# Kernel tuning notes

Measured on AMD Instinct MI355X. Metric: run time of the kernel, lower is better.

Reference implementation:

```python
import jax, jax.numpy as jnp
import numpy as np

N = 20000       # nodes
E = 640000      # random edges (self-loops appended -> E + N total)
G = 64          # graphs in batch
F_IN = 114
H1 = 3          # heads in layer 1
D2 = 128        # output_dim of layer 2
NEG = 0.2       # GATConv leaky_relu negative slope


def setup_inputs() -> dict:
    key = jax.random.key(0)
    ks = jax.random.split(key, 20)
    x = jax.random.normal(ks[0], (N, F_IN), jnp.float32)
    src = jax.random.randint(ks[1], (E,), 0, N, jnp.int32)
    dst = jax.random.randint(ks[2], (E,), 0, N, jnp.int32)
    loop = jnp.arange(N, dtype=jnp.int32)  # PyG add_self_loops=True
    edge_index = jnp.stack([jnp.concatenate([src, loop]),
                            jnp.concatenate([dst, loop])])
    batch = (jnp.arange(N) * G // N).astype(jnp.int32)  # every graph non-empty

    def lin(k, i, o):
        return jax.random.normal(k, (i, o), jnp.float32) * (1.0 / np.sqrt(i))

    return {
        "x": x, "edge_index": edge_index, "batch": batch,
        # GATConv 1: 114 -> 114 per head, 3 heads, concat
        "W1": lin(ks[3], F_IN, H1 * F_IN),
        "a_src1": jax.random.normal(ks[4], (H1, F_IN), jnp.float32) * 0.1,
        "a_dst1": jax.random.normal(ks[5], (H1, F_IN), jnp.float32) * 0.1,
        "b1": jnp.zeros((H1 * F_IN,), jnp.float32),
        # GATConv 2: 342 -> 128, 1 head
        "W2": lin(ks[6], H1 * F_IN, D2),
        "a_src2": jax.random.normal(ks[7], (1, D2), jnp.float32) * 0.1,
        "a_dst2": jax.random.normal(ks[8], (1, D2), jnp.float32) * 0.1,
        "b2": jnp.zeros((D2,), jnp.float32),
        # MLP head
        "Wg": lin(ks[9], D2, 64),  "bg": jnp.zeros((64,), jnp.float32),
        "Wf1": lin(ks[10], 64, 32), "bf1": jnp.zeros((32,), jnp.float32),
        "Wf2": lin(ks[11], 32, 16), "bf2": jnp.zeros((16,), jnp.float32),
        "Wo": lin(ks[12], 16, 1),   "bo": jnp.zeros((1,), jnp.float32),
    }


def gat_conv(x, edge_index, W, a_src, a_dst, b, heads, dim):
    """PyG GATConv (self-loops already in edge_index, eval mode)."""
    n = x.shape[0]
    h = (x @ W).reshape(n, heads, dim)             # [N,H,D]
    src, dst = edge_index[0], edge_index[1]
    alpha_s = jnp.sum(h * a_src, axis=-1)          # [N,H]
    alpha_d = jnp.sum(h * a_dst, axis=-1)          # [N,H]
    e = jax.nn.leaky_relu(alpha_s[src] + alpha_d[dst], NEG)  # [E,H]
    # segment softmax over destination nodes
    m = jax.ops.segment_max(e, dst, num_segments=n)
    ex = jnp.exp(e - m[dst])
    s = jax.ops.segment_sum(ex, dst, num_segments=n)
    alpha = ex / s[dst]                            # [E,H]
    out = jax.ops.segment_sum(h[src] * alpha[..., None], dst, num_segments=n)
    return out.reshape(n, heads * dim) + b


def reference(x, edge_index, batch, W1, a_src1, a_dst1, b1,
              W2, a_src2, a_dst2, b2, Wg, bg, Wf1, bf1, Wf2, bf2, Wo, bo):
    h = jax.nn.elu(gat_conv(x, edge_index, W1, a_src1, a_dst1, b1, H1, F_IN))
    h = jax.nn.relu(gat_conv(h, edge_index, W2, a_src2, a_dst2, b2, 1, D2))
    g = jax.ops.segment_max(h, batch, num_segments=G)   # global max pool [G,128]
    g = jax.nn.relu(g @ Wg + bg)
    g = jax.nn.relu(g @ Wf1 + bf1)
    g = jax.nn.relu(g @ Wf2 + bf2)
    return g @ Wo + bo                                  # [G,1]
```

## Files before the change

### kernel.cpp

```cpp
#include <hip/hip_runtime.h>

#define NN 20000
#define EE 660000
#define GG 64
#define FIN 114
#define H1 3
#define F1 342
#define D2 128
#define NEG 0.2f

__device__ inline unsigned fenc(float f) {
    unsigned u = __float_as_uint(f);
    return (u & 0x80000000u) ? ~u : (u | 0x80000000u);
}
__device__ inline float fdec(unsigned u) {
    return (u & 0x80000000u) ? __uint_as_float(u & 0x7FFFFFFFu) : __uint_as_float(~u);
}
__device__ inline float lrelu(float x) { return x > 0.f ? x : NEG * x; }

__global__ void k_wa(const float* __restrict__ W1, const float* __restrict__ aS,
                     const float* __restrict__ aD, float* __restrict__ was,
                     float* __restrict__ wad) {
    int tid = blockIdx.x * 256 + threadIdx.x;
    if (tid >= 2 * FIN * H1) return;
    int which = tid >= FIN * H1;
    int i = which ? tid - FIN * H1 : tid;
    int k = i / H1, h = i % H1;
    const float* a = which ? aD : aS;
    float s = 0.f;
    for (int d = 0; d < FIN; d++) s += W1[k * F1 + h * FIN + d] * a[h * FIN + d];
    (which ? wad : was)[i] = s;
}

__global__ void k_prep1(const float* __restrict__ W1, float* __restrict__ W1P) {
    int tid = blockIdx.x * 256 + threadIdx.x;
    if (tid >= H1 * 128 * 128) return;
    int h = tid / (128 * 128);
    int rem = tid & (128 * 128 - 1);
    int k = rem >> 7, c = rem & 127;
    W1P[tid] = (c < FIN && k < FIN) ? W1[k * F1 + h * FIN + c] : 0.f;
}

__global__ void k_prep2(const float* __restrict__ W2, float* __restrict__ W2P) {
    int tid = blockIdx.x * 256 + threadIdx.x;
    if (tid >= 3 * 128 * 128) return;
    int hk = tid >> 7, c = tid & 127;
    int h = hk >> 7, k = hk & 127;
    W2P[tid] = (k < FIN) ? W2[(h * FIN + k) * D2 + c] : 0.f;
}

__global__ __launch_bounds__(256) void k_alpha1x(const float* __restrict__ x,
                                                 const float* __restrict__ was,
                                                 const float* __restrict__ wad,
                                                 float* __restrict__ as1,
                                                 float* __restrict__ ad1) {
    int n = blockIdx.x * 4 + (threadIdx.x >> 6);
    int l = threadIdx.x & 63;
    if (n >= NN) return;
    float x0 = x[n * FIN + l];
    float x1 = (l < FIN - 64) ? x[n * FIN + 64 + l] : 0.f;
    float s[H1], d[H1];
#pragma unroll
    for (int h = 0; h < H1; h++) {
        float w0s = was[l * H1 + h], w0d = wad[l * H1 + h];
        float w1s = (l < FIN - 64) ? was[(64 + l) * H1 + h] : 0.f;
        float w1d = (l < FIN - 64) ? wad[(64 + l) * H1 + h] : 0.f;
        s[h] = x0 * w0s + x1 * w1s;
        d[h] = x0 * w0d + x1 * w1d;
    }
#pragma unroll
    for (int o = 32; o > 0; o >>= 1) {
#pragma unroll
        for (int h = 0; h < H1; h++) {
            s[h] += __shfl_down(s[h], o);
            d[h] += __shfl_down(d[h], o);
        }
    }
    if (l == 0) {
#pragma unroll
        for (int h = 0; h < H1; h++) {
            as1[n * H1 + h] = s[h];
            ad1[n * H1 + h] = d[h];
        }
    }
}

__global__ void k_count(const int* __restrict__ dst, int* __restrict__ cnt) {
    int e = blockIdx.x * 256 + threadIdx.x;
    if (e < EE) atomicAdd(&cnt[dst[e]], 1);
}

__global__ __launch_bounds__(1024) void k_scan(const int* __restrict__ cnt,
                                               int* __restrict__ off) {
    __shared__ int part[1024];
    int t = threadIdx.x;
    const int CH = 20;
    int loc[CH];
    int s = 0;
    int base = t * CH;
    for (int i = 0; i < CH; i++) {
        int idx = base + i;
        int v = (idx < NN) ? cnt[idx] : 0;
        loc[i] = s;
        s += v;
    }
    part[t] = s;
    __syncthreads();
    for (int d = 1; d < 1024; d <<= 1) {
        int v = (t >= d) ? part[t - d] : 0;
        __syncthreads();
        part[t] += v;
        __syncthreads();
    }
    int pre = (t == 0) ? 0 : part[t - 1];
    for (int i = 0; i < CH; i++) {
        int idx = base + i;
        if (idx < NN) off[idx] = pre + loc[i];
    }
    if (t == 1023) off[NN] = part[1023];
}

__global__ void k_scatter(const int* __restrict__ src, const int* __restrict__ dst,
                          const int* __restrict__ off, int* __restrict__ cur,
                          int* __restrict__ csr_src) {
    int e = blockIdx.x * 256 + threadIdx.x;
    if (e < EE) {
        int d = dst[e];
        int pos = off[d] + atomicAdd(&cur[d], 1);
        csr_src[pos] = src[e];
    }
}

__global__ __launch_bounds__(128) void k_aggx(const float* __restrict__ x,
                                              const float* __restrict__ as1,
                                              const float* __restrict__ ad1,
                                              const int* __restrict__ off,
                                              const int* __restrict__ csr_src,
                                              float* __restrict__ xaggP) {
    int n = blockIdx.x, t = threadIdx.x;
    int e0 = off[n], e1 = off[n + 1];
    float adv0 = ad1[n * H1 + 0], adv1 = ad1[n * H1 + 1], adv2 = ad1[n * H1 + 2];
    __shared__ int ssrc[64];
    __shared__ float sw[64][H1];
    __shared__ float red[64][H1];
    float acc0 = 0.f, acc1 = 0.f, acc2 = 0.f;
    float ps0 = 0.f, ps1 = 0.f, ps2 = 0.f;
    for (int base = e0; base < e1; base += 64) {
        int c = min(64, e1 - base);
        __syncthreads();
        if (t < c) {
            int s = csr_src[base + t];
            ssrc[t] = s;
            float w0 = __expf(lrelu(as1[s * H1 + 0] + adv0));
            float w1 = __expf(lrelu(as1[s * H1 + 1] + adv1));
            float w2 = __expf(lrelu(as1[s * H1 + 2] + adv2));
            sw[t][0] = w0; sw[t][1] = w1; sw[t][2] = w2;
            ps0 += w0; ps1 += w1; ps2 += w2;
        }
        __syncthreads();
        if (t < FIN) {
            for (int j = 0; j < c; j++) {
                float xv = x[ssrc[j] * FIN + t];
                acc0 += xv * sw[j][0];
                acc1 += xv * sw[j][1];
                acc2 += xv * sw[j][2];
            }
        }
    }
    __syncthreads();
    if (t < 64) { red[t][0] = ps0; red[t][1] = ps1; red[t][2] = ps2; }
    __syncthreads();
    for (int sr = 32; sr > 0; sr >>= 1) {
        if (t < sr) {
            red[t][0] += red[t + sr][0];
            red[t][1] += red[t + sr][1];
            red[t][2] += red[t + sr][2];
        }
        __syncthreads();
    }
    float i0 = 1.f / red[0][0], i1 = 1.f / red[0][1], i2 = 1.f / red[0][2];
    float v0 = (t < FIN) ? acc0 * i0 : 0.f;
    float v1 = (t < FIN) ? acc1 * i1 : 0.f;
    float v2 = (t < FIN) ? acc2 * i2 : 0.f;
    xaggP[(size_t)0 * NN * 128 + n * 128 + t] = v0;
    xaggP[(size_t)1 * NN * 128 + n * 128 + t] = v1;
    xaggP[(size_t)2 * NN * 128 + n * 128 + t] = v2;
}

__global__ __launch_bounds__(256) void k_gemm1t(const float* __restrict__ xaggP,
                                                const float* __restrict__ W1P,
                                                const float* __restrict__ b1,
                                                float* __restrict__ h1aP) {
    int h = blockIdx.y;
    int rb = blockIdx.x * 64;
    int t = threadIdx.x;
    int tr = t >> 4, tc = t & 15;
    __shared__ float As[64][36];
    __shared__ float Bs[32][132];
    const float* Ap = xaggP + (size_t)h * NN * 128;
    const float* Bp = W1P + (size_t)h * 128 * 128;
    const float4 zf4 = make_float4(0.f, 0.f, 0.f, 0.f);

    int ar0 = t >> 3, ak0 = t & 7;
    int ar1 = 32 + ar0;
    int bk[4], bn[4];
#pragma unroll
    for (int q = 0; q < 4; q++) { int idd = t + q * 256; bk[q] = idd >> 5; bn[q] = idd & 31; }

    float4 aR[2], bR[4];
    {
        int g0 = rb + ar0, g1 = rb + ar1;
        aR[0] = (g0 < NN) ? *(const float4*)(Ap + (size_t)g0 * 128 + ak0 * 4) : zf4;
        aR[1] = (g1 < NN) ? *(const float4*)(Ap + (size_t)g1 * 128 + ak0 * 4) : zf4;
#pragma unroll
        for (int q = 0; q < 4; q++)
            bR[q] = *(const float4*)(Bp + (size_t)bk[q] * 128 + bn[q] * 4);
    }
    float acc[4][8] = {};
    for (int tile = 0; tile < 4; tile++) {
        if (tile) __syncthreads();
        *(float4*)(&As[ar0][ak0 * 4]) = aR[0];
        *(float4*)(&As[ar1][ak0 * 4]) = aR[1];
#pragma unroll
        for (int q = 0; q < 4; q++) *(float4*)(&Bs[bk[q]][bn[q] * 4]) = bR[q];
        __syncthreads();
        if (tile < 3) {
            int k0 = (tile + 1) * 32;
            int g0 = rb + ar0, g1 = rb + ar1;
            aR[0] = (g0 < NN) ? *(const float4*)(Ap + (size_t)g0 * 128 + k0 + ak0 * 4) : zf4;
            aR[1] = (g1 < NN) ? *(const float4*)(Ap + (size_t)g1 * 128 + k0 + ak0 * 4) : zf4;
#pragma unroll
            for (int q = 0; q < 4; q++)
                bR[q] = *(const float4*)(Bp + (size_t)(k0 + bk[q]) * 128 + bn[q] * 4);
        }
#pragma unroll
        for (int kc = 0; kc < 32; kc += 4) {
            float a4[4][4];
#pragma unroll
            for (int r = 0; r < 4; r++)
                *(float4*)a4[r] = *(const float4*)(&As[tr * 4 + r][kc]);
#pragma unroll
            for (int kk = 0; kk < 4; kk++) {
                float4 b0 = *(const float4*)(&Bs[kc + kk][tc * 4]);
                float4 b1v = *(const float4*)(&Bs[kc + kk][64 + tc * 4]);
#pragma unroll
                for (int r = 0; r < 4; r++) {
                    float av = a4[r][kk];
                    acc[r][0] += av * b0.x;  acc[r][1] += av * b0.y;
                    acc[r][2] += av * b0.z;  acc[r][3] += av * b0.w;
                    acc[r][4] += av * b1v.x; acc[r][5] += av * b1v.y;
                    acc[r][6] += av * b1v.z; acc[r][7] += av * b1v.w;
                }
            }
        }
    }
    float* Hp = h1aP + (size_t)h * NN * 128;
    int c0 = tc * 4, c1 = 64 + tc * 4;
    float bvA[4], bvB[4];
#pragma unroll
    for (int j = 0; j < 4; j++) {
        bvA[j] = b1[h * FIN + c0 + j];
        bvB[j] = (c1 + j < FIN) ? b1[h * FIN + c1 + j] : 0.f;
    }
#pragma unroll
    for (int r = 0; r < 4; r++) {
        int row = rb + tr * 4 + r;
        if (row >= NN) continue;
        float vA[4], vB[4];
#pragma unroll
        for (int j = 0; j < 4; j++) {
            float v = acc[r][j] + bvA[j];
            vA[j] = v > 0.f ? v : expm1f(v);
            float w = acc[r][j + 4] + bvB[j];
            vB[j] = (c1 + j < FIN) ? (w > 0.f ? w : expm1f(w)) : 0.f;
        }
        *(float4*)(Hp + (size_t)row * 128 + c0) = make_float4(vA[0], vA[1], vA[2], vA[3]);
        *(float4*)(Hp + (size_t)row * 128 + c1) = make_float4(vB[0], vB[1], vB[2], vB[3]);
    }
}

__global__ __launch_bounds__(256) void k_gemm2t(const float* __restrict__ h1aP,
                                                const float* __restrict__ W2P,
                                                float* __restrict__ h2) {
    int mt = blockIdx.x >> 1, nb = (blockIdx.x & 1) * 64;
    int rb = mt * 64;
    int t = threadIdx.x;
    int tr = t >> 4, tc = t & 15;
    __shared__ float As[64][36];
    __shared__ float Bs[32][68];
    const float4 zf4 = make_float4(0.f, 0.f, 0.f, 0.f);
    int ar0 = t >> 3, ak0 = t & 7;
    int ar1 = 32 + ar0;
    int bk0 = t >> 4, bn0 = t & 15;
    int bk1 = 16 + bk0;
    auto loadA = [&](int row, int kg) -> float4 {
        if (row >= NN) return zf4;
        int h = kg >> 7, kc = kg & 127;
        return *(const float4*)(h1aP + ((size_t)h * NN + row) * 128 + kc);
    };
    float4 aR[2], bR[2];
    {
        int g0 = rb + ar0, g1 = rb + ar1;
        aR[0] = loadA(g0, ak0 * 4);
        aR[1] = loadA(g1, ak0 * 4);
        bR[0] = *(const float4*)(W2P + (size_t)bk0 * D2 + nb + bn0 * 4);
        bR[1] = *(const float4*)(W2P + (size_t)bk1 * D2 + nb + bn0 * 4);
    }
    float acc[4][4] = {};
    for (int tile = 0; tile < 12; tile++) {
        if (tile) __syncthreads();
        *(float4*)(&As[ar0][ak0 * 4]) = aR[0];
        *(float4*)(&As[ar1][ak0 * 4]) = aR[1];
        *(float4*)(&Bs[bk0][bn0 * 4]) = bR[0];
        *(float4*)(&Bs[bk1][bn0 * 4]) = bR[1];
        __syncthreads();
        if (tile < 11) {
            int k0 = (tile + 1) * 32;
            int g0 = rb + ar0, g1 = rb + ar1;
            aR[0] = loadA(g0, k0 + ak0 * 4);
            aR[1] = loadA(g1, k0 + ak0 * 4);
            bR[0] = *(const float4*)(W2P + (size_t)(k0 + bk0) * D2 + nb + bn0 * 4);
            bR[1] = *(const float4*)(W2P + (size_t)(k0 + bk1) * D2 + nb + bn0 * 4);
        }
#pragma unroll
        for (int kc = 0; kc < 32; kc += 4) {
            float a4[4][4];
#pragma unroll
            for (int r = 0; r < 4; r++)
                *(float4*)a4[r] = *(const float4*)(&As[tr * 4 + r][kc]);
#pragma unroll
            for (int kk = 0; kk < 4; kk++) {
                float4 b0 = *(const float4*)(&Bs[kc + kk][tc * 4]);
#pragma unroll
                for (int r = 0; r < 4; r++) {
                    float av = a4[r][kk];
                    acc[r][0] += av * b0.x; acc[r][1] += av * b0.y;
                    acc[r][2] += av * b0.z; acc[r][3] += av * b0.w;
                }
            }
        }
    }
#pragma unroll
    for (int r = 0; r < 4; r++) {
        int row = rb + tr * 4 + r;
        if (row < NN)
            *(float4*)(&h2[(size_t)row * D2 + nb + tc * 4]) =
                make_float4(acc[r][0], acc[r][1], acc[r][2], acc[r][3]);
    }
}

__global__ __launch_bounds__(256) void k_alpha2(const float* __restrict__ h2,
                                                const float* __restrict__ aS,
                                                const float* __restrict__ aD,
                                                float* __restrict__ as2,
                                                float* __restrict__ ad2) {
    int n = blockIdx.x * 4 + (threadIdx.x >> 6);
    int l = threadIdx.x & 63;
    if (n >= NN) return;
    float v0 = h2[(size_t)n * D2 + l], v1 = h2[(size_t)n * D2 + 64 + l];
    float ps = v0 * aS[l] + v1 * aS[64 + l];
    float pd = v0 * aD[l] + v1 * aD[64 + l];
    for (int o = 32; o > 0; o >>= 1) {
        ps += __shfl_down(ps, o);
        pd += __shfl_down(pd, o);
    }
    if (l == 0) {
        as2[n] = ps;
        ad2[n] = pd;
    }
}

__global__ __launch_bounds__(128) void k_agg2f(const float* __restrict__ h2,
                                               const float* __restrict__ as2,
                                               const float* __restrict__ ad2,
                                               const int* __restrict__ off,
                                               const int* __restrict__ csr_src,
                                               const float* __restrict__ b2,
                                               unsigned* __restrict__ poolbuf) {
    int n = blockIdx.x, t = threadIdx.x;
    int e0 = off[n], e1 = off[n + 1];
    float adv = ad2[n];
    __shared__ int ssrc[64];
    __shared__ float sw[64];
    __shared__ float red[64];
    float acc = 0.f, ps = 0.f;
    for (int base = e0; base < e1; base += 64) {
        int c = min(64, e1 - base);
        __syncthreads();
        if (t < c) {
            int s = csr_src[base + t];
            ssrc[t] = s;
            float w = __expf(lrelu(as2[s] + adv));
            sw[t] = w;
            ps += w;
        }
        __syncthreads();
        for (int j = 0; j < c; j++) acc += h2[(size_t)ssrc[j] * D2 + t] * sw[j];
    }
    __syncthreads();
    if (t < 64) red[t] = ps;
    __syncthreads();
    for (int sr = 32; sr > 0; sr >>= 1) {
        if (t < sr) red[t] += red[t + sr];
        __syncthreads();
    }
    float v = fmaxf(acc / red[0] + b2[t], 0.f);
    int g = (int)(((long long)n * GG) / NN);
    atomicMax(&poolbuf[g * D2 + t], fenc(v));
}

__global__ __launch_bounds__(128) void k_mlp(const unsigned* __restrict__ poolbuf,
                                             const float* __restrict__ Wg,
                                             const float* __restrict__ bg,
                                             const float* __restrict__ Wf1,
                                             const float* __restrict__ bf1,
                                             const float* __restrict__ Wf2,
                                             const float* __restrict__ bf2,
                                             const float* __restrict__ Wo,
                                             const float* __restrict__ bo,
                                             float* __restrict__ out) {
    int g = blockIdx.x;
    int t = threadIdx.x;
    __shared__ float pool[D2];
    __shared__ float a1[64];
    __shared__ float a2[32];
    __shared__ float a3[16];
    pool[t] = fdec(poolbuf[g * D2 + t]);
    __syncthreads();
    if (t < 64) {
        float acc = bg[t];
        for (int k = 0; k < D2; k++) acc += pool[k] * Wg[k * 64 + t];
        a1[t] = fmaxf(acc, 0.f);
    }
    __syncthreads();
    if (t < 32) {
        float acc = bf1[t];
        for (int k = 0; k < 64; k++) acc += a1[k] * Wf1[k * 32 + t];
        a2[t] = fmaxf(acc, 0.f);
    }
    __syncthreads();
    if (t < 16) {
        float acc = bf2[t];
        for (int k = 0; k < 32; k++) acc += a2[k] * Wf2[k * 16 + t];
        a3[t] = fmaxf(acc, 0.f);
    }
    __syncthreads();
    if (t == 0) {
        float acc = bo[0];
        for (int k = 0; k < 16; k++) acc += a3[k] * Wo[k];
        out[g] = acc;
    }
}

extern "C" void kernel_launch(void* const* d_in, const int* in_sizes, int n_in,
                              void* d_out, int out_size, void* d_ws, size_t ws_size,
                              hipStream_t stream) {
    const float* x = (const float*)d_in[0];
    const int* ei = (const int*)d_in[1];
    const float* W1 = (const float*)d_in[3];
    const float* aS1 = (const float*)d_in[4];
    const float* aD1 = (const float*)d_in[5];
    const float* b1 = (const float*)d_in[6];
    const float* W2 = (const float*)d_in[7];
    const float* aS2 = (const float*)d_in[8];
    const float* aD2 = (const float*)d_in[9];
    const float* b2 = (const float*)d_in[10];
    const float* Wg = (const float*)d_in[11];
    const float* bg = (const float*)d_in[12];
    const float* Wf1 = (const float*)d_in[13];
    const float* bf1 = (const float*)d_in[14];
    const float* Wf2 = (const float*)d_in[15];
    const float* bf2 = (const float*)d_in[16];
    const float* Wo = (const float*)d_in[17];
    const float* bo = (const float*)d_in[18];
    float* out = (float*)d_out;

    const int* src = ei;
    const int* dst = ei + EE;

    char* ws = (char*)d_ws;
    size_t o = 0;
    auto alloc = [&](size_t bytes) -> char* {
        char* p = ws + o;
        o += (bytes + 255) & ~(size_t)255;
        return p;
    };
    float* was = (float*)alloc((size_t)FIN * H1 * 4);
    float* wad = (float*)alloc((size_t)FIN * H1 * 4);
    float* W1P = (float*)alloc((size_t)H1 * 128 * 128 * 4);
    float* W2P = (float*)alloc((size_t)3 * 128 * 128 * 4);
    float* as1 = (float*)alloc((size_t)NN * H1 * 4);
    float* ad1 = (float*)alloc((size_t)NN * H1 * 4);
    int* cnt = (int*)alloc((size_t)NN * 4);
    int* off = (int*)alloc((size_t)(NN + 1) * 4);
    int* cur = (int*)alloc((size_t)NN * 4);
    int* csr_src = (int*)alloc((size_t)EE * 4);
    float* xaggP = (float*)alloc((size_t)H1 * NN * 128 * 4);
    float* h1aP = (float*)alloc((size_t)H1 * NN * 128 * 4);
    float* h2 = (float*)alloc((size_t)NN * D2 * 4);
    float* as2 = (float*)alloc((size_t)NN * 4);
    float* ad2 = (float*)alloc((size_t)NN * 4);
    unsigned* poolbuf = (unsigned*)alloc((size_t)GG * D2 * 4);
    (void)ws_size;

    hipMemsetAsync(cnt, 0, (size_t)NN * 4, stream);
    hipMemsetAsync(cur, 0, (size_t)NN * 4, stream);
    hipMemsetAsync(poolbuf, 0, (size_t)GG * D2 * 4, stream);

    const int EB = (EE + 255) / 256;

    k_wa<<<(2 * FIN * H1 + 255) / 256, 256, 0, stream>>>(W1, aS1, aD1, was, wad);
    k_prep1<<<(H1 * 128 * 128 + 255) / 256, 256, 0, stream>>>(W1, W1P);
    k_prep2<<<(3 * 128 * 128 + 255) / 256, 256, 0, stream>>>(W2, W2P);
    k_alpha1x<<<(NN + 3) / 4, 256, 0, stream>>>(x, was, wad, as1, ad1);
    k_count<<<EB, 256, 0, stream>>>(dst, cnt);
    k_scan<<<1, 1024, 0, stream>>>(cnt, off);
    k_scatter<<<EB, 256, 0, stream>>>(src, dst, off, cur, csr_src);
    k_aggx<<<NN, 128, 0, stream>>>(x, as1, ad1, off, csr_src, xaggP);
    k_gemm1t<<<dim3((NN + 63) / 64, H1), 256, 0, stream>>>(xaggP, W1P, b1, h1aP);
    k_gemm2t<<<((NN + 63) / 64) * 2, 256, 0, stream>>>(h1aP, W2P, h2);
    k_alpha2<<<(NN + 3) / 4, 256, 0, stream>>>(h2, aS2, aD2, as2, ad2);
    k_agg2f<<<NN, 128, 0, stream>>>(h2, as2, ad2, off, csr_src, b2, poolbuf);
    k_mlp<<<GG, 128, 0, stream>>>(poolbuf, Wg, bg, Wf1, bf1, Wf2, bf2, Wo, bo, out);
}
```

Before: 317.4 us.

## Use 8x8 register tiles in GEMMs and split-K the second GEMM

Both dense GEMMs move to 128-thread blocks in which each thread computes an 8x8 output tile. The A tile is stored transposed in shared memory so a row fragment can be read with vector loads. The second GEMM now covers the full 128 output columns per block and splits K into two halves, writing two partial outputs. k_alpha2 sums those partials into h2 before computing the attention logits. The aim is more FMAs per shared-memory load, at the cost of extra partial-buffer traffic, higher register pressure and fewer threads per block.

```diff
diff --git a/kernel.cpp b/kernel.cpp
--- a/kernel.cpp
+++ b/kernel.cpp
@@ -187,7 +187,7 @@
     xaggP[(size_t)2 * NN * 128 + n * 128 + t] = v2;
 }
 
-__global__ __launch_bounds__(256) void k_gemm1t(const float* __restrict__ xaggP,
+__global__ __launch_bounds__(128) void k_gemm1n(const float* __restrict__ xaggP,
                                                 const float* __restrict__ W1P,
                                                 const float* __restrict__ b1,
                                                 float* __restrict__ h1aP) {
@@ -195,169 +195,167 @@
     int rb = blockIdx.x * 64;
     int t = threadIdx.x;
     int tr = t >> 4, tc = t & 15;
-    __shared__ float As[64][36];
-    __shared__ float Bs[32][132];
+    __shared__ float As[16][68];
+    __shared__ float Bs[16][132];
     const float* Ap = xaggP + (size_t)h * NN * 128;
     const float* Bp = W1P + (size_t)h * 128 * 128;
     const float4 zf4 = make_float4(0.f, 0.f, 0.f, 0.f);
-
-    int ar0 = t >> 3, ak0 = t & 7;
-    int ar1 = 32 + ar0;
-    int bk[4], bn[4];
-#pragma unroll
-    for (int q = 0; q < 4; q++) { int idd = t + q * 256; bk[q] = idd >> 5; bn[q] = idd & 31; }
-
+    int ar = t >> 1, aks = (t & 1) * 8;
+    int bkr = t >> 3, bnc = (t & 7) * 16;
     float4 aR[2], bR[4];
     {
-        int g0 = rb + ar0, g1 = rb + ar1;
-        aR[0] = (g0 < NN) ? *(const float4*)(Ap + (size_t)g0 * 128 + ak0 * 4) : zf4;
-        aR[1] = (g1 < NN) ? *(const float4*)(Ap + (size_t)g1 * 128 + ak0 * 4) : zf4;
+        int g = rb + ar;
+        aR[0] = (g < NN) ? *(const float4*)(Ap + (size_t)g * 128 + aks) : zf4;
+        aR[1] = (g < NN) ? *(const float4*)(Ap + (size_t)g * 128 + aks + 4) : zf4;
 #pragma unroll
         for (int q = 0; q < 4; q++)
-            bR[q] = *(const float4*)(Bp + (size_t)bk[q] * 128 + bn[q] * 4);
-    }
-    float acc[4][8] = {};
-    for (int tile = 0; tile < 4; tile++) {
+            bR[q] = *(const float4*)(Bp + (size_t)bkr * 128 + bnc + q * 4);
+    }
+    float acc[8][8] = {};
+    for (int tile = 0; tile < 8; tile++) {
         if (tile) __syncthreads();
-        *(float4*)(&As[ar0][ak0 * 4]) = aR[0];
-        *(float4*)(&As[ar1][ak0 * 4]) = aR[1];
-#pragma unroll
-        for (int q = 0; q < 4; q++) *(float4*)(&Bs[bk[q]][bn[q] * 4]) = bR[q];
-        __syncthreads();
-        if (tile < 3) {
-            int k0 = (tile + 1) * 32;
-            int g0 = rb + ar0, g1 = rb + ar1;
-            aR[0] = (g0 < NN) ? *(const float4*)(Ap + (size_t)g0 * 128 + k0 + ak0 * 4) : zf4;
-            aR[1] = (g1 < NN) ? *(const float4*)(Ap + (size_t)g1 * 128 + k0 + ak0 * 4) : zf4;
+#pragma unroll
+        for (int j = 0; j < 4; j++) {
+            As[aks + j][ar] = ((const float*)&aR[0])[j];
+            As[aks + 4 + j][ar] = ((const float*)&aR[1])[j];
+        }
+#pragma unroll
+        for (int q = 0; q < 4; q++) *(float4*)(&Bs[bkr][bnc + q * 4]) = bR[q];
+        __syncthreads();
+        if (tile < 7) {
+            int k0 = (tile + 1) * 16;
+            int g = rb + ar;
+            aR[0] = (g < NN) ? *(const float4*)(Ap + (size_t)g * 128 + k0 + aks) : zf4;
+            aR[1] = (g < NN) ? *(const float4*)(Ap + (size_t)g * 128 + k0 + aks + 4) : zf4;
 #pragma unroll
             for (int q = 0; q < 4; q++)
-                bR[q] = *(const float4*)(Bp + (size_t)(k0 + bk[q]) * 128 + bn[q] * 4);
-        }
-#pragma unroll
-        for (int kc = 0; kc < 32; kc += 4) {
-            float a4[4][4];
-#pragma unroll
-            for (int r = 0; r < 4; r++)
-                *(float4*)a4[r] = *(const float4*)(&As[tr * 4 + r][kc]);
-#pragma unroll
-            for (int kk = 0; kk < 4; kk++) {
-                float4 b0 = *(const float4*)(&Bs[kc + kk][tc * 4]);
-                float4 b1v = *(const float4*)(&Bs[kc + kk][64 + tc * 4]);
-#pragma unroll
-                for (int r = 0; r < 4; r++) {
-                    float av = a4[r][kk];
-                    acc[r][0] += av * b0.x;  acc[r][1] += av * b0.y;
-                    acc[r][2] += av * b0.z;  acc[r][3] += av * b0.w;
-                    acc[r][4] += av * b1v.x; acc[r][5] += av * b1v.y;
-                    acc[r][6] += av * b1v.z; acc[r][7] += av * b1v.w;
-                }
-            }
+                bR[q] = *(const float4*)(Bp + (size_t)(k0 + bkr) * 128 + bnc + q * 4);
+        }
+#pragma unroll
+        for (int k = 0; k < 16; k++) {
+            float a8[8], b8[8];
+            *(float4*)(a8 + 0) = *(const float4*)(&As[k][tr * 8]);
+            *(float4*)(a8 + 4) = *(const float4*)(&As[k][tr * 8 + 4]);
+            *(float4*)(b8 + 0) = *(const float4*)(&Bs[k][tc * 4]);
+            *(float4*)(b8 + 4) = *(const float4*)(&Bs[k][64 + tc * 4]);
+#pragma unroll
+            for (int r = 0; r < 8; r++)
+#pragma unroll
+                for (int j = 0; j < 8; j++) acc[r][j] += a8[r] * b8[j];
         }
     }
     float* Hp = h1aP + (size_t)h * NN * 128;
     int c0 = tc * 4, c1 = 64 + tc * 4;
-    float bvA[4], bvB[4];
+    float bv[8];
 #pragma unroll
     for (int j = 0; j < 4; j++) {
-        bvA[j] = b1[h * FIN + c0 + j];
-        bvB[j] = (c1 + j < FIN) ? b1[h * FIN + c1 + j] : 0.f;
-    }
-#pragma unroll
-    for (int r = 0; r < 4; r++) {
-        int row = rb + tr * 4 + r;
+        bv[j] = b1[h * FIN + c0 + j];
+        bv[4 + j] = (c1 + j < FIN) ? b1[h * FIN + c1 + j] : 0.f;
+    }
+#pragma unroll
+    for (int r = 0; r < 8; r++) {
+        int row = rb + tr * 8 + r;
         if (row >= NN) continue;
-        float vA[4], vB[4];
-#pragma unroll
-        for (int j = 0; j < 4; j++) {
-            float v = acc[r][j] + bvA[j];
-            vA[j] = v > 0.f ? v : expm1f(v);
-            float w = acc[r][j + 4] + bvB[j];
-            vB[j] = (c1 + j < FIN) ? (w > 0.f ? w : expm1f(w)) : 0.f;
-        }
-        *(float4*)(Hp + (size_t)row * 128 + c0) = make_float4(vA[0], vA[1], vA[2], vA[3]);
-        *(float4*)(Hp + (size_t)row * 128 + c1) = make_float4(vB[0], vB[1], vB[2], vB[3]);
-    }
-}
-
-__global__ __launch_bounds__(256) void k_gemm2t(const float* __restrict__ h1aP,
+        float v[8];
+#pragma unroll
+        for (int j = 0; j < 8; j++) {
+            float w = acc[r][j] + bv[j];
+            w = w > 0.f ? w : expm1f(w);
+            v[j] = ((j < 4) || (c1 + j - 4 < FIN)) ? w : 0.f;
+        }
+        *(float4*)(Hp + (size_t)row * 128 + c0) = make_float4(v[0], v[1], v[2], v[3]);
+        *(float4*)(Hp + (size_t)row * 128 + c1) = make_float4(v[4], v[5], v[6], v[7]);
+    }
+}
+
+__global__ __launch_bounds__(128) void k_gemm2n(const float* __restrict__ h1aP,
                                                 const float* __restrict__ W2P,
-                                                float* __restrict__ h2) {
-    int mt = blockIdx.x >> 1, nb = (blockIdx.x & 1) * 64;
-    int rb = mt * 64;
+                                                float* __restrict__ h2h) {
+    int ks = blockIdx.y;
+    int rb = blockIdx.x * 64;
+    int kbase = ks * 192;
     int t = threadIdx.x;
     int tr = t >> 4, tc = t & 15;
-    __shared__ float As[64][36];
-    __shared__ float Bs[32][68];
+    __shared__ float As[16][68];
+    __shared__ float Bs[16][132];
     const float4 zf4 = make_float4(0.f, 0.f, 0.f, 0.f);
-    int ar0 = t >> 3, ak0 = t & 7;
-    int ar1 = 32 + ar0;
-    int bk0 = t >> 4, bn0 = t & 15;
-    int bk1 = 16 + bk0;
+    int ar = t >> 1, aks = (t & 1) * 8;
+    int bkr = t >> 3, bnc = (t & 7) * 16;
     auto loadA = [&](int row, int kg) -> float4 {
         if (row >= NN) return zf4;
-        int h = kg >> 7, kc = kg & 127;
-        return *(const float4*)(h1aP + ((size_t)h * NN + row) * 128 + kc);
+        int hh = kg >> 7, kc = kg & 127;
+        return *(const float4*)(h1aP + ((size_t)hh * NN + row) * 128 + kc);
     };
-    float4 aR[2], bR[2];
+    float4 aR[2], bR[4];
     {
-        int g0 = rb + ar0, g1 = rb + ar1;
-        aR[0] = loadA(g0, ak0 * 4);
-        aR[1] = loadA(g1, ak0 * 4);
-        bR[0] = *(const float4*)(W2P + (size_t)bk0 * D2 + nb + bn0 * 4);
-        bR[1] = *(const float4*)(W2P + (size_t)bk1 * D2 + nb + bn0 * 4);
-    }
-    float acc[4][4] = {};
+        int g = rb + ar;
+        aR[0] = loadA(g, kbase + aks);
+        aR[1] = loadA(g, kbase + aks + 4);
+#pragma unroll
+        for (int q = 0; q < 4; q++)
+            bR[q] = *(const float4*)(W2P + (size_t)(kbase + bkr) * 128 + bnc + q * 4);
+    }
+    float acc[8][8] = {};
     for (int tile = 0; tile < 12; tile++) {
         if (tile) __syncthreads();
-        *(float4*)(&As[ar0][ak0 * 4]) = aR[0];
-        *(float4*)(&As[ar1][ak0 * 4]) = aR[1];
-        *(float4*)(&Bs[bk0][bn0 * 4]) = bR[0];
-        *(float4*)(&Bs[bk1][bn0 * 4]) = bR[1];
+#pragma unroll
+        for (int j = 0; j < 4; j++) {
+            As[aks + j][ar] = ((const float*)&aR[0])[j];
+            As[aks + 4 + j][ar] = ((const float*)&aR[1])[j];
+        }
+#pragma unroll
+        for (int q = 0; q < 4; q++) *(float4*)(&Bs[bkr][bnc + q * 4]) = bR[q];
         __syncthreads();
         if (tile < 11) {
-            int k0 = (tile + 1) * 32;
-            int g0 = rb + ar0, g1 = rb + ar1;
-            aR[0] = loadA(g0, k0 + ak0 * 4);
-            aR[1] = loadA(g1, k0 + ak0 * 4);
-            bR[0] = *(const float4*)(W2P + (size_t)(k0 + bk0) * D2 + nb + bn0 * 4);
-            bR[1] = *(const float4*)(W2P + (size_t)(k0 + bk1) * D2 + nb + bn0 * 4);
-        }
-#pragma unroll
-        for (int kc = 0; kc < 32; kc += 4) {
-            float a4[4][4];
-#pragma unroll
-            for (int r = 0; r < 4; r++)
-                *(float4*)a4[r] = *(const float4*)(&As[tr * 4 + r][kc]);
-#pragma unroll
-            for (int kk = 0; kk < 4; kk++) {
-                float4 b0 = *(const float4*)(&Bs[kc + kk][tc * 4]);
-#pragma unroll
-                for (int r = 0; r < 4; r++) {
-                    float av = a4[r][kk];
-                    acc[r][0] += av * b0.x; acc[r][1] += av * b0.y;
-                    acc[r][2] += av * b0.z; acc[r][3] += av * b0.w;
-                }
-            }
-        }
-    }
-#pragma unroll
-    for (int r = 0; r < 4; r++) {
-        int row = rb + tr * 4 + r;
-        if (row < NN)
-            *(float4*)(&h2[(size_t)row * D2 + nb + tc * 4]) =
-                make_float4(acc[r][0], acc[r][1], acc[r][2], acc[r][3]);
-    }
-}
-
-__global__ __launch_bounds__(256) void k_alpha2(const float* __restrict__ h2,
+            int k0 = kbase + (tile + 1) * 16;
+            int g = rb + ar;
+            aR[0] = loadA(g, k0 + aks);
+            aR[1] = loadA(g, k0 + aks + 4);
+#pragma unroll
+            for (int q = 0; q < 4; q++)
+                bR[q] = *(const float4*)(W2P + (size_t)(k0 + bkr) * 128 + bnc + q * 4);
+        }
+#pragma unroll
+        for (int k = 0; k < 16; k++) {
+            float a8[8], b8[8];
+            *(float4*)(a8 + 0) = *(const float4*)(&As[k][tr * 8]);
+            *(float4*)(a8 + 4) = *(const float4*)(&As[k][tr * 8 + 4]);
+            *(float4*)(b8 + 0) = *(const float4*)(&Bs[k][tc * 4]);
+            *(float4*)(b8 + 4) = *(const float4*)(&Bs[k][64 + tc * 4]);
+#pragma unroll
+            for (int r = 0; r < 8; r++)
+#pragma unroll
+                for (int j = 0; j < 8; j++) acc[r][j] += a8[r] * b8[j];
+        }
+    }
+    float* Hp = h2h + (size_t)ks * NN * 128;
+    int c0 = tc * 4, c1 = 64 + tc * 4;
+#pragma unroll
+    for (int r = 0; r < 8; r++) {
+        int row = rb + tr * 8 + r;
+        if (row >= NN) continue;
+        *(float4*)(Hp + (size_t)row * 128 + c0) =
+            make_float4(acc[r][0], acc[r][1], acc[r][2], acc[r][3]);
+        *(float4*)(Hp + (size_t)row * 128 + c1) =
+            make_float4(acc[r][4], acc[r][5], acc[r][6], acc[r][7]);
+    }
+}
+
+__global__ __launch_bounds__(256) void k_alpha2(const float* __restrict__ h2h,
                                                 const float* __restrict__ aS,
                                                 const float* __restrict__ aD,
+                                                float* __restrict__ h2,
                                                 float* __restrict__ as2,
                                                 float* __restrict__ ad2) {
     int n = blockIdx.x * 4 + (threadIdx.x >> 6);
     int l = threadIdx.x & 63;
     if (n >= NN) return;
-    float v0 = h2[(size_t)n * D2 + l], v1 = h2[(size_t)n * D2 + 64 + l];
+    const float* pa = h2h + (size_t)n * D2;
+    const float* pb = h2h + (size_t)NN * D2 + (size_t)n * D2;
+    float v0 = pa[l] + pb[l];
+    float v1 = pa[64 + l] + pb[64 + l];
+    h2[(size_t)n * D2 + l] = v0;
+    h2[(size_t)n * D2 + 64 + l] = v1;
     float ps = v0 * aS[l] + v1 * aS[64 + l];
     float pd = v0 * aD[l] + v1 * aD[64 + l];
     for (int o = 32; o > 0; o >>= 1) {
@@ -497,6 +495,7 @@
     int* csr_src = (int*)alloc((size_t)EE * 4);
     float* xaggP = (float*)alloc((size_t)H1 * NN * 128 * 4);
     float* h1aP = (float*)alloc((size_t)H1 * NN * 128 * 4);
+    float* h2h = (float*)alloc((size_t)2 * NN * D2 * 4);
     float* h2 = (float*)alloc((size_t)NN * D2 * 4);
     float* as2 = (float*)alloc((size_t)NN * 4);
     float* ad2 = (float*)alloc((size_t)NN * 4);
@@ -517,9 +516,9 @@
     k_scan<<<1, 1024, 0, stream>>>(cnt, off);
     k_scatter<<<EB, 256, 0, stream>>>(src, dst, off, cur, csr_src);
     k_aggx<<<NN, 128, 0, stream>>>(x, as1, ad1, off, csr_src, xaggP);
-    k_gemm1t<<<dim3((NN + 63) / 64, H1), 256, 0, stream>>>(xaggP, W1P, b1, h1aP);
-    k_gemm2t<<<((NN + 63) / 64) * 2, 256, 0, stream>>>(h1aP, W2P, h2);
-    k_alpha2<<<(NN + 3) / 4, 256, 0, stream>>>(h2, aS2, aD2, as2, ad2);
+    k_gemm1n<<<dim3((NN + 63) / 64, H1), 128, 0, stream>>>(xaggP, W1P, b1, h1aP);
+    k_gemm2n<<<dim3((NN + 63) / 64, 2), 128, 0, stream>>>(h1aP, W2P, h2h);
+    k_alpha2<<<(NN + 3) / 4, 256, 0, stream>>>(h2h, aS2, aD2, h2, as2, ad2);
     k_agg2f<<<NN, 128, 0, stream>>>(h2, as2, ad2, off, csr_src, b2, poolbuf);
     k_mlp<<<GG, 128, 0, stream>>>(poolbuf, Wg, bg, Wf1, bf1, Wf2, bf2, Wo, bo, out);
 }
```

Result: slower. 341.6 us (+7.6%).
